# Optimization experiments

Measured on AMD Instinct MI355X. Metric: run time of the kernel, lower is better.

The kernel has to match this reference:

```python
import jax, jax.numpy as jnp
import numpy as np

K = 32          # num_cones
D = 512         # decoder feature dim (feature_mapper in_features)
VOX = 32 * 32 * 32
N = 524288      # query points
EPS = 1e-8

CONE_ADDER = jnp.array([-0.8, -0.8, -0.8, 0.05, 0.1, -1.0, -1.0, -1.0], jnp.float32)
CONE_MULT = jnp.array([1.0, 1.0, 1.0, 0.01, 0.03, 1.7, 1.7, 1.7], jnp.float32)


def setup_inputs() -> dict:
    key = jax.random.key(0)
    ks = jax.random.split(key, 8)
    return {
        "voxel_data": jax.random.normal(ks[0], (1, VOX), jnp.float32),
        "query_points": jax.random.uniform(ks[1], (N, 3), jnp.float32, minval=-1.0, maxval=1.0),
        "initial_centers": jax.random.normal(ks[2], (K, 3), jnp.float32) * 0.3,
        # learned params (encoder MLP -> 512, decoder MLP 512->512, feature_mapper 512->K*8)
        "W_enc": jax.random.normal(ks[3], (VOX, D), jnp.float32) * 0.01,
        "b_enc": jnp.zeros((D,), jnp.float32),
        "W_dec": jax.random.normal(ks[4], (D, D), jnp.float32) * 0.04,
        "b_dec": jnp.zeros((D,), jnp.float32),
        "W_map": jax.random.normal(ks[5], (D, K * 8), jnp.float32) * 0.04,
        "b_map": jnp.zeros((K * 8,), jnp.float32),
    }


def determine_cone_sdf(q, p):
    # q: [N,3] query points; p: [K,8] = center(3), radius, height, orientation(3)
    centers = p[:, 0:3]            # [K,3]
    radii = p[:, 3]                # [K]
    heights = p[:, 4]              # [K]
    orient = p[:, 5:8]             # [K,3]
    axis = orient / (jnp.linalg.norm(orient, axis=-1, keepdims=True) + EPS)  # [K,3]
    v = q[:, None, :] - centers[None, :, :]                # [N,K,3]
    proj = jnp.einsum("nkd,kd->nk", v, axis)               # signed dist along axis [N,K]
    perp = jnp.linalg.norm(v - proj[..., None] * axis[None, :, :], axis=-1)  # [N,K]
    # lateral (slanted) surface: radius tapers linearly from base (proj=0) to apex (proj=height)
    slant = perp - radii[None, :] * (1.0 - proj / (heights[None, :] + EPS))
    cap = jnp.abs(proj) - heights[None, :]                 # end caps
    return jnp.maximum(slant, cap)                         # [N,K]


def reference(voxel_data, query_points, initial_centers,
              W_enc, b_enc, W_dec, b_dec, W_map, b_map):
    # encoder (global feature) -> decoder -> feature_mapper
    feat = jax.nn.relu(voxel_data @ W_enc + b_enc)     # [1, D]
    dec = jax.nn.relu(feat @ W_dec + b_dec)            # [1, D]
    cone_params = (dec @ W_map + b_map).reshape(K, 8)  # [K, 8]
    # sigmoid + affine rescale into valid geometric ranges
    cone_params = jax.nn.sigmoid(cone_params) * CONE_MULT + CONE_ADDER
    cone_sdf = determine_cone_sdf(query_points, cone_params)  # [N, K]
    return cone_sdf, cone_params
```

## Files before the change

### kernel.cpp

```cpp
#include <hip/hip_runtime.h>
#include <math.h>

#define DD 512
#define KC 32
#define NQ 524288
#define EPSF 1e-8f
#define CONE_STRIDE 13

typedef float f4 __attribute__((ext_vector_type(4)));

__device__ __constant__ float c_mult[8]  = {1.f, 1.f, 1.f, 0.01f, 0.03f, 1.7f, 1.7f, 1.7f};
__device__ __constant__ float c_adder[8] = {-0.8f, -0.8f, -0.8f, 0.05f, 0.1f, -1.f, -1.f, -1.f};

__global__ __launch_bounds__(512) void k_enc(const float* __restrict__ vox,
                                             const float* __restrict__ Wenc,
                                             float* __restrict__ partialT) {
    __shared__ float4 red4[512];
    const int t = threadIdx.x;
    const int b = blockIdx.x;
    const int g  = t >> 7;
    const int c4 = (t & 127) << 2;
    const int v0 = b * 64;
    float4 acc = make_float4(0.f, 0.f, 0.f, 0.f);
    #pragma unroll
    for (int it = 0; it < 16; ++it) {
        const int v = v0 + it * 4 + g;
        const float sv = vox[v];
        const float4 w = *reinterpret_cast<const float4*>(&Wenc[(size_t)v * DD + c4]);
        acc.x += sv * w.x; acc.y += sv * w.y; acc.z += sv * w.z; acc.w += sv * w.w;
    }
    red4[t] = acc;
    __syncthreads();
    const float* red = reinterpret_cast<const float*>(red4);
    const float s = red[t] + red[512 + t] + red[1024 + t] + red[1536 + t];
    partialT[(size_t)t * 512 + b] = s;
}

__global__ __launch_bounds__(512) void k_dec(const float* __restrict__ partialT,
                                             const float* __restrict__ benc,
                                             const float* __restrict__ Wdec,
                                             float* __restrict__ decPart) {
    __shared__ float4 red4[512];
    __shared__ float wsum[8];
    const int t = threadIdx.x;
    const int g = t >> 7;
    const int j = t & 127;
    const int i = blockIdx.x * 4 + g;
    const float4 pv = *reinterpret_cast<const float4*>(&partialT[(size_t)i * 512 + j * 4]);
    float s = pv.x + pv.y + pv.z + pv.w;
    #pragma unroll
    for (int off = 32; off >= 1; off >>= 1) s += __shfl_xor(s, off, 64);
    if ((t & 63) == 0) wsum[t >> 6] = s;
    __syncthreads();
    float fi = wsum[2 * g] + wsum[2 * g + 1] + benc[i];
    fi = fi > 0.f ? fi : 0.f;
    const float4 w = *reinterpret_cast<const float4*>(&Wdec[(size_t)i * DD + (j << 2)]);
    red4[t] = make_float4(fi * w.x, fi * w.y, fi * w.z, fi * w.w);
    __syncthreads();
    const float* red = reinterpret_cast<const float*>(red4);
    const float s2 = red[t] + red[512 + t] + red[1024 + t] + red[1536 + t];
    decPart[(size_t)blockIdx.x * 512 + t] = s2;
}

__global__ __launch_bounds__(512) void k_map(const float* __restrict__ decPart,
                                             const float* __restrict__ bdec,
                                             const float* __restrict__ Wmap,
                                             float* __restrict__ mapPart) {
    __shared__ float dec8[8];
    __shared__ float half0[256];
    const int t = threadIdx.x;
    const int b = blockIdx.x;
    const int w = t >> 6, l = t & 63;
    const int i = b * 8 + w;
    float s = decPart[(size_t)(2 * l) * 512 + i] + decPart[(size_t)(2 * l + 1) * 512 + i];
    #pragma unroll
    for (int off = 32; off >= 1; off >>= 1) s += __shfl_xor(s, off, 64);
    if (l == 0) {
        const float d = s + bdec[i];
        dec8[w] = d > 0.f ? d : 0.f;
    }
    __syncthreads();
    const int j = t & 255, h = t >> 8;
    float acc = 0.f;
    #pragma unroll
    for (int r = 0; r < 4; ++r) {
        const int row = h * 4 + r;
        acc += dec8[row] * Wmap[(size_t)(b * 8 + row) * 256 + j];
    }
    if (h == 0) half0[j] = acc;
    __syncthreads();
    if (h == 1) mapPart[(size_t)b * 256 + j] = half0[j] + acc;
}

__global__ __launch_bounds__(256) void k_params(const float* __restrict__ mapPart,
                                                const float* __restrict__ bmap,
                                                float* __restrict__ out_params,
                                                float* __restrict__ cones) {
    __shared__ float p[256];
    const int j = threadIdx.x;
    float m = 0.f;
    #pragma unroll 8
    for (int pi = 0; pi < 64; ++pi) m += mapPart[(size_t)pi * 256 + j];
    const float tot = m + bmap[j];
    const float sig = 1.f / (1.f + expf(-tot));
    const float val = sig * c_mult[j & 7] + c_adder[j & 7];
    out_params[j] = val;
    p[j] = val;
    __syncthreads();
    if (j < KC) {
        const float cx = p[j*8+0], cy = p[j*8+1], cz = p[j*8+2];
        const float r  = p[j*8+3], hh = p[j*8+4];
        const float ox = p[j*8+5], oy = p[j*8+6], oz = p[j*8+7];
        const float nrm = sqrtf(ox*ox + oy*oy + oz*oz) + EPSF;
        const float inv = 1.f / nrm;
        const float inv_h = 1.f / (hh + EPSF);
        float* ck = &cones[j * CONE_STRIDE];
        ck[0] = cx;        ck[1] = cy;       ck[2] = cz;
        ck[3] = ox * inv;  ck[4] = oy * inv; ck[5] = oz * inv;
        ck[6] = r;         ck[7] = hh;       ck[8] = inv_h;
        ck[9] = r * inv_h; ck[10] = 0.f;     ck[11] = 0.f;  ck[12] = 0.f;
    }
}

__global__ __launch_bounds__(256) void k_sdf(const float* __restrict__ q,
                                             const float* __restrict__ cones,
                                             float* __restrict__ out) {
    __shared__ float c[KC * CONE_STRIDE];
    const int t = threadIdx.x;
    c[t] = cones[t];
    if (t < KC * CONE_STRIDE - 256) c[256 + t] = cones[256 + t];
    __syncthreads();
    const int k0 = (t & 7) << 2;
    float cx[4], cy[4], cz[4], ax[4], ay[4], az[4], cr[4], chh[4], rih[4];
    #pragma unroll
    for (int kk = 0; kk < 4; ++kk) {
        const float* ck = &c[(k0 + kk) * CONE_STRIDE];
        cx[kk] = ck[0]; cy[kk] = ck[1]; cz[kk] = ck[2];
        ax[kk] = ck[3]; ay[kk] = ck[4]; az[kk] = ck[5];
        cr[kk] = ck[6]; chh[kk] = ck[7]; rih[kk] = ck[9];
    }
    const size_t qbase = (size_t)blockIdx.x * 256;
    const int nl = t >> 3;
    #pragma unroll
    for (int tile = 0; tile < 8; ++tile) {
        const size_t n = qbase + tile * 32 + nl;
        const float qx = q[n * 3 + 0];
        const float qy = q[n * 3 + 1];
        const float qz = q[n * 3 + 2];
        f4 o;
        #pragma unroll
        for (int kk = 0; kk < 4; ++kk) {
            const float vx = qx - cx[kk];
            const float vy = qy - cy[kk];
            const float vz = qz - cz[kk];
            const float proj = vx*ax[kk] + vy*ay[kk] + vz*az[kk];
            const float d2 = vx*vx + vy*vy + vz*vz;
            float pp = d2 - proj * proj;
            pp = pp > 0.f ? pp : 0.f;
            const float perp = sqrtf(pp);
            const float slant = perp - cr[kk] + rih[kk] * proj;
            const float cap = fabsf(proj) - chh[kk];
            o[kk] = slant > cap ? slant : cap;
        }
        __builtin_nontemporal_store(o, reinterpret_cast<f4*>(&out[n * (size_t)KC + k0]));
    }
}

extern "C" void kernel_launch(void* const* d_in, const int* in_sizes, int n_in,
                              void* d_out, int out_size, void* d_ws, size_t ws_size,
                              hipStream_t stream) {
    const float* vox  = (const float*)d_in[0];
    const float* q    = (const float*)d_in[1];
    const float* Wenc = (const float*)d_in[3];
    const float* benc = (const float*)d_in[4];
    const float* Wdec = (const float*)d_in[5];
    const float* bdec = (const float*)d_in[6];
    const float* Wmap = (const float*)d_in[7];
    const float* bmap = (const float*)d_in[8];
    float* out = (float*)d_out;
    float* ws  = (float*)d_ws;

    float* partialT = ws;
    float *decPart, *mapPart, *cones;
    const size_t fullF = 262144 + 65536 + 16384 + 512;
    if (ws_size >= fullF * sizeof(float)) {
        decPart = ws + 262144;
        mapPart = decPart + 65536;
        cones   = mapPart + 16384;
    } else {
        decPart = out;
        mapPart = out + 65536;
        cones   = ws + 262144;
    }
    float* out_params = out + (size_t)NQ * KC;

    k_enc<<<512, 512, 0, stream>>>(vox, Wenc, partialT);
    k_dec<<<128, 512, 0, stream>>>(partialT, benc, Wdec, decPart);
    k_map<<<64, 512, 0, stream>>>(decPart, bdec, Wmap, mapPart);
    k_params<<<1, 256, 0, stream>>>(mapPart, bmap, out_params, cones);
    k_sdf<<<2048, 256, 0, stream>>>(q, cones, out);
}
```

Baseline: 45.64 us.

## Fuse encoder/decoder/mapper/param kernels into one cooperative kernel with grid syncs

```diff
diff --git a/kernel.cpp b/kernel.cpp
--- a/kernel.cpp
+++ b/kernel.cpp
@@ -1,5 +1,8 @@
 #include <hip/hip_runtime.h>
+#include <hip/hip_cooperative_groups.h>
 #include <math.h>
+
+namespace cg = cooperative_groups;
 
 #define DD 512
 #define KC 32
@@ -12,6 +15,120 @@
 __device__ __constant__ float c_mult[8]  = {1.f, 1.f, 1.f, 0.01f, 0.03f, 1.7f, 1.7f, 1.7f};
 __device__ __constant__ float c_adder[8] = {-0.8f, -0.8f, -0.8f, 0.05f, 0.1f, -1.f, -1.f, -1.f};
 
+__global__ __launch_bounds__(512, 4) void k_mid(
+        const float* __restrict__ vox,  const float* __restrict__ Wenc,
+        const float* __restrict__ benc, const float* __restrict__ Wdec,
+        const float* __restrict__ bdec, const float* __restrict__ Wmap,
+        const float* __restrict__ bmap,
+        float* __restrict__ partialT,   float* __restrict__ decPart,
+        float* __restrict__ mapPart,    float* __restrict__ out_params,
+        float* __restrict__ cones) {
+    cg::grid_group grid = cg::this_grid();
+    __shared__ float4 red4[512];
+    __shared__ float wsum[8];
+    __shared__ float dec8[8];
+    __shared__ float half0[256];
+    __shared__ float pbuf[256];
+    const int t = threadIdx.x;
+    const int b = blockIdx.x;
+
+    #pragma unroll
+    for (int chunk = 0; chunk < 2; ++chunk) {
+        const int bb = b * 2 + chunk;
+        const int g  = t >> 7;
+        const int c4 = (t & 127) << 2;
+        const int v0 = bb * 64;
+        float4 acc = make_float4(0.f, 0.f, 0.f, 0.f);
+        #pragma unroll
+        for (int it = 0; it < 16; ++it) {
+            const int v = v0 + it * 4 + g;
+            const float sv = vox[v];
+            const float4 w = *reinterpret_cast<const float4*>(&Wenc[(size_t)v * DD + c4]);
+            acc.x += sv * w.x; acc.y += sv * w.y; acc.z += sv * w.z; acc.w += sv * w.w;
+        }
+        __syncthreads();
+        red4[t] = acc;
+        __syncthreads();
+        const float* red = reinterpret_cast<const float*>(red4);
+        partialT[(size_t)t * 512 + bb] = red[t] + red[512 + t] + red[1024 + t] + red[1536 + t];
+    }
+    grid.sync();
+
+    if (b < 128) {
+        const int g = t >> 7;
+        const int j = t & 127;
+        const int i = b * 4 + g;
+        const float4 pv = *reinterpret_cast<const float4*>(&partialT[(size_t)i * 512 + j * 4]);
+        float s = pv.x + pv.y + pv.z + pv.w;
+        #pragma unroll
+        for (int off = 32; off >= 1; off >>= 1) s += __shfl_xor(s, off, 64);
+        if ((t & 63) == 0) wsum[t >> 6] = s;
+        __syncthreads();
+        float fi = wsum[2 * g] + wsum[2 * g + 1] + benc[i];
+        fi = fi > 0.f ? fi : 0.f;
+        const float4 w = *reinterpret_cast<const float4*>(&Wdec[(size_t)i * DD + (j << 2)]);
+        red4[t] = make_float4(fi * w.x, fi * w.y, fi * w.z, fi * w.w);
+        __syncthreads();
+        const float* red = reinterpret_cast<const float*>(red4);
+        decPart[(size_t)b * 512 + t] = red[t] + red[512 + t] + red[1024 + t] + red[1536 + t];
+    }
+    grid.sync();
+
+    if (b < 64) {
+        const int w = t >> 6, l = t & 63;
+        const int i = b * 8 + w;
+        float s = decPart[(size_t)(2 * l) * 512 + i] + decPart[(size_t)(2 * l + 1) * 512 + i];
+        #pragma unroll
+        for (int off = 32; off >= 1; off >>= 1) s += __shfl_xor(s, off, 64);
+        if (l == 0) {
+            const float d = s + bdec[i];
+            dec8[w] = d > 0.f ? d : 0.f;
+        }
+        __syncthreads();
+        const int j = t & 255, h = t >> 8;
+        float acc = 0.f;
+        #pragma unroll
+        for (int r = 0; r < 4; ++r) {
+            const int row = h * 4 + r;
+            acc += dec8[row] * Wmap[(size_t)(b * 8 + row) * 256 + j];
+        }
+        if (h == 0) half0[j] = acc;
+        __syncthreads();
+        if (h == 1) mapPart[(size_t)b * 256 + j] = half0[j] + acc;
+    }
+    grid.sync();
+
+    if (b == 0) {
+        const int j = t & 255, h = t >> 8;
+        float m = 0.f;
+        #pragma unroll 8
+        for (int pi = h * 32; pi < h * 32 + 32; ++pi) m += mapPart[(size_t)pi * 256 + j];
+        if (h == 0) half0[j] = m;
+        __syncthreads();
+        if (h == 1) {
+            const float tot = half0[j] + m + bmap[j];
+            const float sig = 1.f / (1.f + expf(-tot));
+            const float val = sig * c_mult[j & 7] + c_adder[j & 7];
+            pbuf[j] = val;
+            out_params[j] = val;
+        }
+        __syncthreads();
+        if (t < KC) {
+            const float cx = pbuf[t*8+0], cy = pbuf[t*8+1], cz = pbuf[t*8+2];
+            const float r  = pbuf[t*8+3], hh = pbuf[t*8+4];
+            const float ox = pbuf[t*8+5], oy = pbuf[t*8+6], oz = pbuf[t*8+7];
+            const float nrm = sqrtf(ox*ox + oy*oy + oz*oz) + EPSF;
+            const float inv = 1.f / nrm;
+            const float inv_h = 1.f / (hh + EPSF);
+            float* ck = &cones[t * CONE_STRIDE];
+            ck[0] = cx;        ck[1] = cy;       ck[2] = cz;
+            ck[3] = ox * inv;  ck[4] = oy * inv; ck[5] = oz * inv;
+            ck[6] = r;         ck[7] = hh;       ck[8] = inv_h;
+            ck[9] = r * inv_h; ck[10] = 0.f;     ck[11] = 0.f;  ck[12] = 0.f;
+        }
+    }
+}
+
 __global__ __launch_bounds__(512) void k_enc(const float* __restrict__ vox,
                                              const float* __restrict__ Wenc,
                                              float* __restrict__ partialT) {
@@ -32,8 +149,7 @@
     red4[t] = acc;
     __syncthreads();
     const float* red = reinterpret_cast<const float*>(red4);
-    const float s = red[t] + red[512 + t] + red[1024 + t] + red[1536 + t];
-    partialT[(size_t)t * 512 + b] = s;
+    partialT[(size_t)t * 512 + b] = red[t] + red[512 + t] + red[1024 + t] + red[1536 + t];
 }
 
 __global__ __launch_bounds__(512) void k_dec(const float* __restrict__ partialT,
@@ -58,8 +174,7 @@
     red4[t] = make_float4(fi * w.x, fi * w.y, fi * w.z, fi * w.w);
     __syncthreads();
     const float* red = reinterpret_cast<const float*>(red4);
-    const float s2 = red[t] + red[512 + t] + red[1024 + t] + red[1536 + t];
-    decPart[(size_t)blockIdx.x * 512 + t] = s2;
+    decPart[(size_t)blockIdx.x * 512 + t] = red[t] + red[512 + t] + red[1024 + t] + red[1536 + t];
 }
 
 __global__ __launch_bounds__(512) void k_map(const float* __restrict__ decPart,
@@ -194,9 +309,27 @@
     }
     float* out_params = out + (size_t)NQ * KC;
 
-    k_enc<<<512, 512, 0, stream>>>(vox, Wenc, partialT);
-    k_dec<<<128, 512, 0, stream>>>(partialT, benc, Wdec, decPart);
-    k_map<<<64, 512, 0, stream>>>(decPart, bdec, Wmap, mapPart);
-    k_params<<<1, 256, 0, stream>>>(mapPart, bmap, out_params, cones);
+    int dev = 0;  hipGetDevice(&dev);
+    int numCU = 0;
+    hipDeviceGetAttribute(&numCU, hipDeviceAttributeMultiprocessorCount, dev);
+    int maxB = 0;
+    hipOccupancyMaxActiveBlocksPerMultiprocessor(&maxB, k_mid, 512, 0);
+
+    bool coop = (numCU > 0) && ((long)maxB * numCU >= 256);
+    if (coop) {
+        void* args[] = { (void*)&vox, (void*)&Wenc, (void*)&benc, (void*)&Wdec,
+                         (void*)&bdec, (void*)&Wmap, (void*)&bmap,
+                         (void*)&partialT, (void*)&decPart, (void*)&mapPart,
+                         (void*)&out_params, (void*)&cones };
+        hipError_t err = hipLaunchCooperativeKernel((const void*)k_mid, dim3(256),
+                                                    dim3(512), args, 0, stream);
+        if (err != hipSuccess) coop = false;
+    }
+    if (!coop) {
+        k_enc<<<512, 512, 0, stream>>>(vox, Wenc, partialT);
+        k_dec<<<128, 512, 0, stream>>>(partialT, benc, Wdec, decPart);
+        k_map<<<64, 512, 0, stream>>>(decPart, bdec, Wmap, mapPart);
+        k_params<<<1, 256, 0, stream>>>(mapPart, bmap, out_params, cones);
+    }
     k_sdf<<<2048, 256, 0, stream>>>(q, cones, out);
 }
```

After: 148.1 us. +224.4%, slower.

## Fuse map and params kernels, prefetch weights and query points into L2

Applied to the files above, without the earlier changes.

```diff
diff --git a/kernel.cpp b/kernel.cpp
--- a/kernel.cpp
+++ b/kernel.cpp
@@ -14,10 +14,18 @@
 
 __global__ __launch_bounds__(512) void k_enc(const float* __restrict__ vox,
                                              const float* __restrict__ Wenc,
+                                             const float* __restrict__ Wdec,
+                                             const float* __restrict__ Wmap,
                                              float* __restrict__ partialT) {
     __shared__ float4 red4[512];
     const int t = threadIdx.x;
     const int b = blockIdx.x;
+    f4 pf = {0.f, 0.f, 0.f, 0.f};
+    const int idx = b * 512 + t;
+    if (idx < 65536 + 32768) {
+        pf = (idx < 65536) ? reinterpret_cast<const f4*>(Wdec)[idx]
+                           : reinterpret_cast<const f4*>(Wmap)[idx - 65536];
+    }
     const int g  = t >> 7;
     const int c4 = (t & 127) << 2;
     const int v0 = b * 64;
@@ -33,7 +41,8 @@
     __syncthreads();
     const float* red = reinterpret_cast<const float*>(red4);
     const float s = red[t] + red[512 + t] + red[1024 + t] + red[1536 + t];
-    partialT[(size_t)t * 512 + b] = s;
+    partialT[(size_t)b * 512 + t] = s;
+    asm volatile("" :: "v"(pf.x), "v"(pf.y));
 }
 
 __global__ __launch_bounds__(512) void k_dec(const float* __restrict__ partialT,
@@ -46,8 +55,10 @@
     const int g = t >> 7;
     const int j = t & 127;
     const int i = blockIdx.x * 4 + g;
-    const float4 pv = *reinterpret_cast<const float4*>(&partialT[(size_t)i * 512 + j * 4]);
-    float s = pv.x + pv.y + pv.z + pv.w;
+    float s = 0.f;
+    #pragma unroll
+    for (int m = 0; m < 4; ++m)
+        s += partialT[(size_t)(j + 128 * m) * 512 + i];
     #pragma unroll
     for (int off = 32; off >= 1; off >>= 1) s += __shfl_xor(s, off, 64);
     if ((t & 63) == 0) wsum[t >> 6] = s;
@@ -62,59 +73,89 @@
     decPart[(size_t)blockIdx.x * 512 + t] = s2;
 }
 
-__global__ __launch_bounds__(512) void k_map(const float* __restrict__ decPart,
-                                             const float* __restrict__ bdec,
-                                             const float* __restrict__ Wmap,
-                                             float* __restrict__ mapPart) {
-    __shared__ float dec8[8];
-    __shared__ float half0[256];
+__global__ __launch_bounds__(512) void k_cones(const float* __restrict__ decPart,
+                                               const float* __restrict__ bdec,
+                                               const float* __restrict__ Wmap,
+                                               const float* __restrict__ bmap,
+                                               const float* __restrict__ q,
+                                               float* __restrict__ out_params,
+                                               float* __restrict__ cones,
+                                               float* __restrict__ qsink) {
     const int t = threadIdx.x;
     const int b = blockIdx.x;
-    const int w = t >> 6, l = t & 63;
-    const int i = b * 8 + w;
-    float s = decPart[(size_t)(2 * l) * 512 + i] + decPart[(size_t)(2 * l + 1) * 512 + i];
-    #pragma unroll
-    for (int off = 32; off >= 1; off >>= 1) s += __shfl_xor(s, off, 64);
-    if (l == 0) {
-        const float d = s + bdec[i];
-        dec8[w] = d > 0.f ? d : 0.f;
-    }
-    __syncthreads();
-    const int j = t & 255, h = t >> 8;
-    float acc = 0.f;
-    #pragma unroll
-    for (int r = 0; r < 4; ++r) {
-        const int row = h * 4 + r;
-        acc += dec8[row] * Wmap[(size_t)(b * 8 + row) * 256 + j];
-    }
-    if (h == 0) half0[j] = acc;
-    __syncthreads();
-    if (h == 1) mapPart[(size_t)b * 256 + j] = half0[j] + acc;
-}
-
-__global__ __launch_bounds__(256) void k_params(const float* __restrict__ mapPart,
-                                                const float* __restrict__ bmap,
-                                                float* __restrict__ out_params,
-                                                float* __restrict__ cones) {
-    __shared__ float p[256];
-    const int j = threadIdx.x;
-    float m = 0.f;
-    #pragma unroll 8
-    for (int pi = 0; pi < 64; ++pi) m += mapPart[(size_t)pi * 256 + j];
-    const float tot = m + bmap[j];
-    const float sig = 1.f / (1.f + expf(-tot));
-    const float val = sig * c_mult[j & 7] + c_adder[j & 7];
-    out_params[j] = val;
-    p[j] = val;
-    __syncthreads();
-    if (j < KC) {
-        const float cx = p[j*8+0], cy = p[j*8+1], cz = p[j*8+2];
-        const float r  = p[j*8+3], hh = p[j*8+4];
-        const float ox = p[j*8+5], oy = p[j*8+6], oz = p[j*8+7];
+    if (b >= 8) {
+        const f4* q4 = reinterpret_cast<const f4*>(q);
+        f4 acc = {0.f, 0.f, 0.f, 0.f};
+        const int nth = 248 * 512;
+        for (int i = (b - 8) * 512 + t; i < (NQ * 3) / 4; i += nth) {
+            f4 v = q4[i];
+            acc.x += v.x; acc.y += v.y; acc.z += v.z; acc.w += v.w;
+        }
+        if (t == 0) qsink[b] = acc.x + acc.y + acc.z + acc.w;
+        return;
+    }
+    __shared__ f4 red[512];
+    __shared__ float dec_lds[DD];
+    __shared__ float psum[512];
+    __shared__ float pbuf[32];
+    {
+        const f4* dP4 = reinterpret_cast<const f4*>(decPart);
+        const int d4 = t & 127;
+        const int bc = t >> 7;
+        f4 a = {0.f, 0.f, 0.f, 0.f};
+        #pragma unroll
+        for (int m = 0; m < 32; ++m) {
+            const f4 v = dP4[(size_t)(bc * 32 + m) * 128 + d4];
+            a.x += v.x; a.y += v.y; a.z += v.z; a.w += v.w;
+        }
+        red[t] = a;
+        __syncthreads();
+        if (t < 128) {
+            f4 s = red[t];
+            const f4 s1 = red[t + 128], s2 = red[t + 256], s3 = red[t + 384];
+            s.x += s1.x + s2.x + s3.x; s.y += s1.y + s2.y + s3.y;
+            s.z += s1.z + s2.z + s3.z; s.w += s1.w + s2.w + s3.w;
+            const f4 bd = reinterpret_cast<const f4*>(bdec)[t];
+            dec_lds[4*t+0] = fmaxf(s.x + bd.x, 0.f);
+            dec_lds[4*t+1] = fmaxf(s.y + bd.y, 0.f);
+            dec_lds[4*t+2] = fmaxf(s.z + bd.z, 0.f);
+            dec_lds[4*t+3] = fmaxf(s.w + bd.w, 0.f);
+        }
+        __syncthreads();
+    }
+    {
+        const int jj = t & 31;
+        const int c  = t >> 5;
+        const int j  = b * 32 + jj;
+        float acc = 0.f;
+        #pragma unroll
+        for (int r = 0; r < 32; ++r) {
+            const int i = c * 32 + r;
+            acc += dec_lds[i] * Wmap[(size_t)i * 256 + j];
+        }
+        psum[c * 32 + jj] = acc;
+        __syncthreads();
+        if (t < 32) {
+            float m = 0.f;
+            #pragma unroll
+            for (int cc = 0; cc < 16; ++cc) m += psum[cc * 32 + t];
+            const float tot = m + bmap[b * 32 + t];
+            const float sig = 1.f / (1.f + expf(-tot));
+            const float val = sig * c_mult[t & 7] + c_adder[t & 7];
+            out_params[b * 32 + t] = val;
+            pbuf[t] = val;
+        }
+        __syncthreads();
+    }
+    if (t < 4) {
+        const float* p = &pbuf[t * 8];
+        const float cx = p[0], cy = p[1], cz = p[2];
+        const float r  = p[3], hh = p[4];
+        const float ox = p[5], oy = p[6], oz = p[7];
         const float nrm = sqrtf(ox*ox + oy*oy + oz*oz) + EPSF;
         const float inv = 1.f / nrm;
         const float inv_h = 1.f / (hh + EPSF);
-        float* ck = &cones[j * CONE_STRIDE];
+        float* ck = &cones[(b * 4 + t) * CONE_STRIDE];
         ck[0] = cx;        ck[1] = cy;       ck[2] = cz;
         ck[3] = ox * inv;  ck[4] = oy * inv; ck[5] = oz * inv;
         ck[6] = r;         ck[7] = hh;       ck[8] = inv_h;
@@ -181,22 +222,22 @@
     float* ws  = (float*)d_ws;
 
     float* partialT = ws;
-    float *decPart, *mapPart, *cones;
-    const size_t fullF = 262144 + 65536 + 16384 + 512;
+    float *decPart, *cones, *qsink;
+    const size_t fullF = 262144 + 65536 + 512 + 256;
     if (ws_size >= fullF * sizeof(float)) {
         decPart = ws + 262144;
-        mapPart = decPart + 65536;
-        cones   = mapPart + 16384;
+        cones   = decPart + 65536;
+        qsink   = cones + 512;
     } else {
         decPart = out;
-        mapPart = out + 65536;
         cones   = ws + 262144;
+        qsink   = cones + 512;
     }
     float* out_params = out + (size_t)NQ * KC;
 
-    k_enc<<<512, 512, 0, stream>>>(vox, Wenc, partialT);
+    k_enc<<<512, 512, 0, stream>>>(vox, Wenc, Wdec, Wmap, partialT);
     k_dec<<<128, 512, 0, stream>>>(partialT, benc, Wdec, decPart);
-    k_map<<<64, 512, 0, stream>>>(decPart, bdec, Wmap, mapPart);
-    k_params<<<1, 256, 0, stream>>>(mapPart, bmap, out_params, cones);
+    k_cones<<<256, 512, 0, stream>>>(decPart, bdec, Wmap, bmap, q,
+                                     out_params, cones, qsink);
     k_sdf<<<2048, 256, 0, stream>>>(q, cones, out);
 }
```

Result: no change. 45.39 us (-0.5%).
